# Optimization experiments

Hardware: AMD Instinct MI355X
Metric: run time of the kernel (lower is better)

Reference implementation:

```python
import jax, jax.numpy as jnp
import numpy as np

H = 768   # hidden_dim * SMPL_NR_JOINTS = 32 * 24
O = 72    # output_dim * SMPL_NR_JOINTS = 3 * 24
B = 256
T = 100   # max_len (tgt.size(1))
SRC_LEN = 16


def setup_inputs() -> dict:
    key = jax.random.key(0)
    ks = jax.random.split(key, 10)
    s = 1.0 / np.sqrt(H)
    return {
        "src": jax.random.normal(ks[0], (B, SRC_LEN, H), jnp.float32),
        "tgt": jax.random.normal(ks[1], (B, T, O), jnp.float32),
        "h0": jax.random.normal(ks[2], (B, H), jnp.float32),
        "c0": jax.random.normal(ks[3], (B, H), jnp.float32),
        "W_ih": jax.random.uniform(ks[4], (4 * H, H), jnp.float32, -s, s),
        "W_hh": jax.random.uniform(ks[5], (4 * H, H), jnp.float32, -s, s),
        "b_ih": jax.random.uniform(ks[6], (4 * H,), jnp.float32, -s, s),
        "b_hh": jax.random.uniform(ks[7], (4 * H,), jnp.float32, -s, s),
        "W_post": jax.random.uniform(ks[8], (O, H), jnp.float32, -s, s),
        "b_post": jax.random.uniform(ks[9], (O,), jnp.float32, -s, s),
    }


def reference(src, tgt, h0, c0, W_ih, W_hh, b_ih, b_hh, W_post, b_post):
    max_len = tgt.shape[1]
    bias = b_ih + b_hh  # [4H]

    def step(carry, _):
        x, h, c = carry  # each [B, H]
        gates = x @ W_ih.T + h @ W_hh.T + bias  # [B, 4H]
        i, f, g, o = jnp.split(gates, 4, axis=-1)  # PyTorch gate order i,f,g,o
        c = jax.nn.sigmoid(f) * c + jax.nn.sigmoid(i) * jnp.tanh(g)
        h = jax.nn.sigmoid(o) * jnp.tanh(c)
        return (h, h, c), h  # decoder output feeds back as next input

    x0 = src[:, -1]  # out = src[:, -1].unsqueeze(1)
    _, outs = jax.lax.scan(step, (x0, h0, c0), None, length=max_len)  # [T, B, H]
    outs = jnp.transpose(outs, (1, 0, 2))  # [B, T, H]
    return outs @ W_post.T + b_post  # [B, T, O]
```

## Files before the change

### kernel.cpp

```cpp
#include <hip/hip_runtime.h>
#include <hip/hip_bf16.h>
#include <math.h>

#define H 768
#define B 256
#define T 100

typedef __attribute__((ext_vector_type(8))) short short8;
typedef __attribute__((ext_vector_type(4))) float f32x4;
typedef unsigned long long u64;

static __device__ __forceinline__ float sigm(float x) {
    return 1.0f / (1.0f + __expf(-x));
}
static __device__ __forceinline__ float tanh_fast(float x) {
    return 1.0f - 2.0f / (__expf(2.0f * x) + 1.0f);
}

__global__ void prep_all(const float* __restrict__ src, const float* __restrict__ h0,
                         const float* __restrict__ Wih, const float* __restrict__ Whh,
                         const float* __restrict__ bih, const float* __restrict__ bhh,
                         const float* __restrict__ Wpost,
                         __hip_bfloat16* __restrict__ Wc,
                         __hip_bfloat16* __restrict__ Wcat,
                         float* __restrict__ bias,
                         __hip_bfloat16* __restrict__ Wp,
                         __hip_bfloat16* __restrict__ A0,
                         u64* __restrict__ sig64)
{
    const int bx = blockIdx.x;
    const int y  = blockIdx.y;
    const int k  = bx * 256 + threadIdx.x;
    if (y < 3072) {
        float a = Wih[y * H + k];
        float b = Whh[y * H + k];
        Wc[y * H + k] = __float2bfloat16(a + b);
        Wcat[y * 1536 + k] = __float2bfloat16(a);
        Wcat[y * 1536 + H + k] = __float2bfloat16(b);
        if (bx == 0 && threadIdx.x == 0) bias[y] = bih[y] + bhh[y];
    } else if (y < 3152) {
        int r = y - 3072;
        Wp[r * H + k] = (r < 72) ? __float2bfloat16(Wpost[r * H + k])
                                 : __float2bfloat16(0.0f);
    } else if (y < 3408) {
        int b = y - 3152;
        A0[b * 1536 + k] = __float2bfloat16(src[(b * 16 + 15) * H + k]);
        A0[b * 1536 + H + k] = __float2bfloat16(h0[b * H + k]);
    } else {
        sig64[(size_t)(y - 3408) * 768 + k] = 0ull;
    }
}

#define LDS_H_STRIDE  772
#define LDS_T0_STRIDE 1540
#define XCH_STRIDE    17

#define LDW(nm, idx) \
    asm volatile("global_load_dwordx4 %0, %1, off" \
                 : "=v"(nm) : "v"(wptr + (idx) * 32))

#define KSTEP(nm, idx) { \
    short8 a_ = *(const short8*)(&lds_h[col * LDS_H_STRIDE + (idx) * 32 + quad * 8]); \
    acc = __builtin_amdgcn_mfma_f32_16x16x32_bf16(a_, nm, acc, 0, 0, 0); }

static __device__ __forceinline__ bool sig_ok(u64 x) {
    return (unsigned short)x && (unsigned short)(x >> 16) &&
           (unsigned short)(x >> 32) && (unsigned short)(x >> 48);
}

__global__ __launch_bounds__(768, 3) void lstm_persist(
    const __hip_bfloat16* __restrict__ Wc,
    const __hip_bfloat16* __restrict__ Wcat,
    const float* __restrict__ bias,
    const float* __restrict__ c0in,
    const __hip_bfloat16* __restrict__ A0,
    unsigned* sig)
{
    const int mtg  = blockIdx.x >> 4;
    const int jg   = blockIdx.x & 15;
    const int tid  = threadIdx.x;
    const int lane = tid & 63;
    const int wave = tid >> 6;
    const int col  = lane & 15;
    const int quad = lane >> 4;
    const int jt_l = wave >> 2;
    const int gate = wave & 3;
    const int j    = jg * 48 + jt_l * 16 + col;

    __shared__ short lds_h[16 * LDS_T0_STRIDE];
    __shared__ float xch[12 * 16 * XCH_STRIDE];

    const short* wptr = (const short*)Wc + (size_t)(gate * H + j) * H + quad * 8;
    short8 w00,w01,w02,w03,w04,w05,w06,w07,w08,w09,w10,w11,
           w12,w13,w14,w15,w16,w17,w18,w19,w20,w21,w22,w23;
    LDW(w00,0);  LDW(w01,1);  LDW(w02,2);  LDW(w03,3);
    LDW(w04,4);  LDW(w05,5);  LDW(w06,6);  LDW(w07,7);
    LDW(w08,8);  LDW(w09,9);  LDW(w10,10); LDW(w11,11);
    LDW(w12,12); LDW(w13,13); LDW(w14,14); LDW(w15,15);
    LDW(w16,16); LDW(w17,17); LDW(w18,18); LDW(w19,19);
    LDW(w20,20); LDW(w21,21); LDW(w22,22); LDW(w23,23);
    asm volatile("s_waitcnt vmcnt(0)" ::: "memory");

    const int p    = tid;
    const int bb   = p / 24;
    const int jp   = p % 24;
    const int jloc = jp * 2;
    const int cjt  = jloc >> 4;
    const int jcol = jloc & 15;
    const int bglob = mtg * 16 + bb;
    const int jglob = jg * 48 + jloc;
    float c0v = 0.f, c1v = 0.f;
    float bi0=0,bi1=0,bf0=0,bf1=0,bg0=0,bg1=0,bo0=0,bo1=0;
    if (p < 384) {
        c0v = c0in[(size_t)bglob * H + jglob];
        c1v = c0in[(size_t)bglob * H + jglob + 1];
        bi0 = bias[0*H + jglob]; bi1 = bias[0*H + jglob + 1];
        bf0 = bias[1*H + jglob]; bf1 = bias[1*H + jglob + 1];
        bg0 = bias[2*H + jglob]; bg1 = bias[2*H + jglob + 1];
        bo0 = bias[3*H + jglob]; bo1 = bias[3*H + jglob + 1];
    }

    const u64* sig64c = (const u64*)sig;
    const int r0  = tid / 192;
    const int wrd = tid % 192;

    for (int t = 0; t < T; ++t) {
        f32x4 acc = {0.f, 0.f, 0.f, 0.f};

        if (t == 0) {
            const u64* a8 = (const u64*)((const short*)A0 + (size_t)(mtg * 16) * 1536);
#pragma unroll
            for (int i = 0; i < 8; ++i) {
                int idx = tid + i * 768;
                int br  = idx / 384;
                int ch  = idx % 384;
                *(u64*)&lds_h[br * LDS_T0_STRIDE + ch * 4] = a8[(size_t)br * 384 + ch];
            }
            __syncthreads();

            const short* wq = (const short*)Wcat + (size_t)(gate * H + j) * 1536 + quad * 8;
            for (int kk = 0; kk < 48; ++kk) {
                short8 a_ = *(const short8*)(&lds_h[col * LDS_T0_STRIDE + kk * 32 + quad * 8]);
                short8 b_ = *(const short8*)(wq + kk * 32);
                acc = __builtin_amdgcn_mfma_f32_16x16x32_bf16(a_, b_, acc, 0, 0, 0);
            }
        } else {
            const u64* hb = sig64c + ((size_t)(t - 1) * B + (size_t)(mtg * 16)) * 192;
            unsigned pending = 0xFu;
#pragma unroll
            for (int i = 0; i < 4; ++i) {
                int row = r0 + 4 * i;
                u64 x = __hip_atomic_load(hb + (size_t)row * 192 + wrd,
                                          __ATOMIC_RELAXED, __HIP_MEMORY_SCOPE_AGENT);
                if (sig_ok(x)) {
                    *(u64*)&lds_h[row * LDS_H_STRIDE + wrd * 4] = ~x;
                    pending &= ~(1u << i);
                }
            }
            int guard = 0;
            while (pending && ++guard < (1 << 22)) {
                __builtin_amdgcn_s_sleep(1);
#pragma unroll
                for (int i = 0; i < 4; ++i) {
                    if (pending & (1u << i)) {
                        int row = r0 + 4 * i;
                        u64 x = __hip_atomic_load(hb + (size_t)row * 192 + wrd,
                                                  __ATOMIC_RELAXED, __HIP_MEMORY_SCOPE_AGENT);
                        if (sig_ok(x)) {
                            *(u64*)&lds_h[row * LDS_H_STRIDE + wrd * 4] = ~x;
                            pending &= ~(1u << i);
                        }
                    }
                }
            }
            __syncthreads();

            KSTEP(w00,0)  KSTEP(w01,1)  KSTEP(w02,2)  KSTEP(w03,3)
            KSTEP(w04,4)  KSTEP(w05,5)  KSTEP(w06,6)  KSTEP(w07,7)
            KSTEP(w08,8)  KSTEP(w09,9)  KSTEP(w10,10) KSTEP(w11,11)
            KSTEP(w12,12) KSTEP(w13,13) KSTEP(w14,14) KSTEP(w15,15)
            KSTEP(w16,16) KSTEP(w17,17) KSTEP(w18,18) KSTEP(w19,19)
            KSTEP(w20,20) KSTEP(w21,21) KSTEP(w22,22) KSTEP(w23,23)
        }

        float* xw = &xch[(size_t)wave * 16 * XCH_STRIDE];
#pragma unroll
        for (int r = 0; r < 4; ++r)
            xw[(quad * 4 + r) * XCH_STRIDE + col] = acc[r];
        __syncthreads();

        if (p < 384) {
            const float* xg = &xch[(size_t)(cjt * 4) * 16 * XCH_STRIDE + bb * XCH_STRIDE + jcol];
            const int gs = 16 * XCH_STRIDE;
            float i0 = xg[0*gs] + bi0, i1 = xg[0*gs + 1] + bi1;
            float f0 = xg[1*gs] + bf0, f1 = xg[1*gs + 1] + bf1;
            float g0 = xg[2*gs] + bg0, g1 = xg[2*gs + 1] + bg1;
            float o0 = xg[3*gs] + bo0, o1 = xg[3*gs + 1] + bo1;
            float cn0 = sigm(f0) * c0v + sigm(i0) * tanh_fast(g0);
            float cn1 = sigm(f1) * c1v + sigm(i1) * tanh_fast(g1);
            c0v = cn0; c1v = cn1;
            __hip_bfloat16 h0b = __float2bfloat16(sigm(o0) * tanh_fast(cn0));
            __hip_bfloat16 h1b = __float2bfloat16(sigm(o1) * tanh_fast(cn1));
            unsigned lo = (unsigned)(unsigned short)~(*(unsigned short*)&h0b);
            unsigned hi = (unsigned)(unsigned short)~(*(unsigned short*)&h1b);
            __hip_atomic_store(&sig[((size_t)t * B + bglob) * 384 + (jglob >> 1)],
                               lo | (hi << 16),
                               __ATOMIC_RELAXED, __HIP_MEMORY_SCOPE_AGENT);
        }

        __syncthreads();
    }
}

__global__ __launch_bounds__(64) void proj(
    const short* __restrict__ Hs,
    const __hip_bfloat16* __restrict__ Wp,
    const float* __restrict__ bpost,
    float* __restrict__ out)
{
    const int mt = blockIdx.x;
    const int lane = threadIdx.x;
    const int col = lane & 15;
    const int quad = lane >> 4;

    const short* Ap = Hs + (size_t)(mt * 16 + col) * H + quad * 8;
    const short* Wb = (const short*)Wp;

    f32x4 acc[5];
#pragma unroll
    for (int nt = 0; nt < 5; ++nt) acc[nt] = (f32x4){0.f, 0.f, 0.f, 0.f};

    for (int k = 0; k < H; k += 32) {
        short8 a = ~(*(const short8*)(Ap + k));
#pragma unroll
        for (int nt = 0; nt < 5; ++nt) {
            short8 b = *(const short8*)(Wb + (size_t)(nt * 16 + col) * H + quad * 8 + k);
            acc[nt] = __builtin_amdgcn_mfma_f32_16x16x32_bf16(a, b, acc[nt], 0, 0, 0);
        }
    }

#pragma unroll
    for (int nt = 0; nt < 5; ++nt) {
        const int o = nt * 16 + col;
        if (o < 72) {
            const float bb = bpost[o];
#pragma unroll
            for (int r = 0; r < 4; ++r) {
                const int m = mt * 16 + quad * 4 + r;
                const int t = m >> 8;
                const int b = m & 255;
                out[((size_t)b * T + t) * 72 + o] = acc[nt][r] + bb;
            }
        }
    }
}


extern "C" void kernel_launch(void* const* d_in, const int* in_sizes, int n_in,
                              void* d_out, int out_size, void* d_ws, size_t ws_size,
                              hipStream_t stream) {
    const float* src   = (const float*)d_in[0];
    const float* h0    = (const float*)d_in[2];
    const float* c0    = (const float*)d_in[3];
    const float* Wih   = (const float*)d_in[4];
    const float* Whh   = (const float*)d_in[5];
    const float* bih   = (const float*)d_in[6];
    const float* bhh   = (const float*)d_in[7];
    const float* Wpost = (const float*)d_in[8];
    const float* bpost = (const float*)d_in[9];
    float* out = (float*)d_out;

    char* ws = (char*)d_ws;
    __hip_bfloat16* Wcat = (__hip_bfloat16*)(ws + 0);
    __hip_bfloat16* Wc   = (__hip_bfloat16*)(ws + 9437184);
    float*          bias = (float*)(ws + 14155776);
    __hip_bfloat16* Wp   = (__hip_bfloat16*)(ws + 14168064);
    __hip_bfloat16* A0   = (__hip_bfloat16*)(ws + 14290944);
    unsigned*       sig  = (unsigned*)(ws + 15863808);

    prep_all<<<dim3(3, 9808), 256, 0, stream>>>(src, h0, Wih, Whh, bih, bhh, Wpost,
                                                Wc, Wcat, bias, Wp, A0, (u64*)sig);

    lstm_persist<<<256, 768, 0, stream>>>(Wc, Wcat, bias, c0, A0, sig);

    proj<<<1600, 64, 0, stream>>>((const short*)sig, Wp, bpost, out);
}
```

Baseline: 500.2 us.

## Switch persistent LSTM to 32x32 MFMA tiles with 192-thread blocks

Reworks the persistent LSTM kernel to use 32x32x16 bf16 MFMA instead of 16x16x32. Each block now covers 32 batch rows by 24 hidden units across all four gates using 3 waves, in place of 16 rows by 48 units with 12 waves, and each wave keeps 48 register-resident weight fragments. The cell update now handles 4 batch rows per thread and packs neighbouring outputs with a lane shuffle, and the trailing barrier per step is dropped. This aims to cut per-step MFMA issue and synchronisation overhead, at the cost of higher register pressure, fewer waves per CU and more spin-poll loads per thread. The removed barrier could also let the next step's LDS writes race with reads still in progress.

```diff
diff --git a/kernel.cpp b/kernel.cpp
--- a/kernel.cpp
+++ b/kernel.cpp
@@ -7,6 +7,7 @@
 #define T 100
 
 typedef __attribute__((ext_vector_type(8))) short short8;
+typedef __attribute__((ext_vector_type(16))) float f32x16;
 typedef __attribute__((ext_vector_type(4))) float f32x4;
 typedef unsigned long long u64;
 
@@ -53,22 +54,32 @@
 
 #define LDS_H_STRIDE  772
 #define LDS_T0_STRIDE 1540
-#define XCH_STRIDE    17
-
-#define LDW(nm, idx) \
-    asm volatile("global_load_dwordx4 %0, %1, off" \
-                 : "=v"(nm) : "v"(wptr + (idx) * 32))
-
-#define KSTEP(nm, idx) { \
-    short8 a_ = *(const short8*)(&lds_h[col * LDS_H_STRIDE + (idx) * 32 + quad * 8]); \
-    acc = __builtin_amdgcn_mfma_f32_16x16x32_bf16(a_, nm, acc, 0, 0, 0); }
+#define XCH_STRIDE    33
+
+#define LDW8(n0,n1,n2,n3,n4,n5,n6,n7, p) \
+    asm volatile("global_load_dwordx4 %0, %8, off\n\t" \
+                 "global_load_dwordx4 %1, %8, off offset:32\n\t" \
+                 "global_load_dwordx4 %2, %8, off offset:64\n\t" \
+                 "global_load_dwordx4 %3, %8, off offset:96\n\t" \
+                 "global_load_dwordx4 %4, %8, off offset:128\n\t" \
+                 "global_load_dwordx4 %5, %8, off offset:160\n\t" \
+                 "global_load_dwordx4 %6, %8, off offset:192\n\t" \
+                 "global_load_dwordx4 %7, %8, off offset:224\n\t" \
+                 "s_waitcnt vmcnt(0)" \
+                 : "=&v"(n0),"=&v"(n1),"=&v"(n2),"=&v"(n3), \
+                   "=&v"(n4),"=&v"(n5),"=&v"(n6),"=&v"(n7) \
+                 : "v"(p))
+
+#define KST(nm, idx) { \
+    short8 a_ = *(const short8*)(&lds_h[arow * LDS_H_STRIDE + (idx) * 16 + half * 8]); \
+    acc = __builtin_amdgcn_mfma_f32_32x32x16_bf16(a_, nm, acc, 0, 0, 0); }
 
 static __device__ __forceinline__ bool sig_ok(u64 x) {
     return (unsigned short)x && (unsigned short)(x >> 16) &&
            (unsigned short)(x >> 32) && (unsigned short)(x >> 48);
 }
 
-__global__ __launch_bounds__(768, 3) void lstm_persist(
+__global__ __launch_bounds__(192, 1) void lstm_persist(
     const __hip_bfloat16* __restrict__ Wc,
     const __hip_bfloat16* __restrict__ Wcat,
     const float* __restrict__ bias,
@@ -76,84 +87,79 @@
     const __hip_bfloat16* __restrict__ A0,
     unsigned* sig)
 {
-    const int mtg  = blockIdx.x >> 4;
-    const int jg   = blockIdx.x & 15;
+    const int mtg  = blockIdx.x >> 5;
+    const int jg   = blockIdx.x & 31;
     const int tid  = threadIdx.x;
     const int lane = tid & 63;
     const int wave = tid >> 6;
-    const int col  = lane & 15;
-    const int quad = lane >> 4;
-    const int jt_l = wave >> 2;
-    const int gate = wave & 3;
-    const int j    = jg * 48 + jt_l * 16 + col;
-
-    __shared__ short lds_h[16 * LDS_T0_STRIDE];
-    __shared__ float xch[12 * 16 * XCH_STRIDE];
-
-    const short* wptr = (const short*)Wc + (size_t)(gate * H + j) * H + quad * 8;
+    const int arow = lane & 31;
+    const int half = lane >> 5;
+    const int r    = wave * 32 + arow;
+    const int g    = r / 24;
+    const int j_l  = r % 24;
+    const int Wrow = g * H + jg * 24 + j_l;
+
+    __shared__ short lds_h[32 * LDS_T0_STRIDE];
+    __shared__ float xch[96 * XCH_STRIDE];
+
+    const short* wptr = (const short*)Wc + (size_t)Wrow * H + half * 8;
     short8 w00,w01,w02,w03,w04,w05,w06,w07,w08,w09,w10,w11,
-           w12,w13,w14,w15,w16,w17,w18,w19,w20,w21,w22,w23;
-    LDW(w00,0);  LDW(w01,1);  LDW(w02,2);  LDW(w03,3);
-    LDW(w04,4);  LDW(w05,5);  LDW(w06,6);  LDW(w07,7);
-    LDW(w08,8);  LDW(w09,9);  LDW(w10,10); LDW(w11,11);
-    LDW(w12,12); LDW(w13,13); LDW(w14,14); LDW(w15,15);
-    LDW(w16,16); LDW(w17,17); LDW(w18,18); LDW(w19,19);
-    LDW(w20,20); LDW(w21,21); LDW(w22,22); LDW(w23,23);
-    asm volatile("s_waitcnt vmcnt(0)" ::: "memory");
-
-    const int p    = tid;
-    const int bb   = p / 24;
-    const int jp   = p % 24;
-    const int jloc = jp * 2;
-    const int cjt  = jloc >> 4;
-    const int jcol = jloc & 15;
-    const int bglob = mtg * 16 + bb;
-    const int jglob = jg * 48 + jloc;
-    float c0v = 0.f, c1v = 0.f;
-    float bi0=0,bi1=0,bf0=0,bf1=0,bg0=0,bg1=0,bo0=0,bo1=0;
-    if (p < 384) {
-        c0v = c0in[(size_t)bglob * H + jglob];
-        c1v = c0in[(size_t)bglob * H + jglob + 1];
-        bi0 = bias[0*H + jglob]; bi1 = bias[0*H + jglob + 1];
-        bf0 = bias[1*H + jglob]; bf1 = bias[1*H + jglob + 1];
-        bg0 = bias[2*H + jglob]; bg1 = bias[2*H + jglob + 1];
-        bo0 = bias[3*H + jglob]; bo1 = bias[3*H + jglob + 1];
-    }
+           w12,w13,w14,w15,w16,w17,w18,w19,w20,w21,w22,w23,
+           w24,w25,w26,w27,w28,w29,w30,w31,w32,w33,w34,w35,
+           w36,w37,w38,w39,w40,w41,w42,w43,w44,w45,w46,w47;
+    LDW8(w00,w01,w02,w03,w04,w05,w06,w07, wptr);
+    LDW8(w08,w09,w10,w11,w12,w13,w14,w15, wptr + 128);
+    LDW8(w16,w17,w18,w19,w20,w21,w22,w23, wptr + 256);
+    LDW8(w24,w25,w26,w27,w28,w29,w30,w31, wptr + 384);
+    LDW8(w32,w33,w34,w35,w36,w37,w38,w39, wptr + 512);
+    LDW8(w40,w41,w42,w43,w44,w45,w46,w47, wptr + 640);
+
+    const int cj   = tid % 24;
+    const int cb   = tid / 24;
+    const int jglob = jg * 24 + cj;
+    const int bglob0 = mtg * 32 + cb * 4;
+    const float bi = bias[0 * H + jglob];
+    const float bf = bias[1 * H + jglob];
+    const float bg = bias[2 * H + jglob];
+    const float bo = bias[3 * H + jglob];
+    float cv[4];
+#pragma unroll
+    for (int rr = 0; rr < 4; ++rr)
+        cv[rr] = c0in[(size_t)(bglob0 + rr) * H + jglob];
 
     const u64* sig64c = (const u64*)sig;
-    const int r0  = tid / 192;
-    const int wrd = tid % 192;
 
     for (int t = 0; t < T; ++t) {
-        f32x4 acc = {0.f, 0.f, 0.f, 0.f};
+        f32x16 acc;
+#pragma unroll
+        for (int i = 0; i < 16; ++i) acc[i] = 0.f;
 
         if (t == 0) {
-            const u64* a8 = (const u64*)((const short*)A0 + (size_t)(mtg * 16) * 1536);
-#pragma unroll
-            for (int i = 0; i < 8; ++i) {
-                int idx = tid + i * 768;
+            const u64* a8 = (const u64*)((const short*)A0 + (size_t)(mtg * 32) * 1536);
+#pragma unroll
+            for (int i = 0; i < 64; ++i) {
+                int idx = tid + i * 192;
                 int br  = idx / 384;
                 int ch  = idx % 384;
                 *(u64*)&lds_h[br * LDS_T0_STRIDE + ch * 4] = a8[(size_t)br * 384 + ch];
             }
             __syncthreads();
 
-            const short* wq = (const short*)Wcat + (size_t)(gate * H + j) * 1536 + quad * 8;
-            for (int kk = 0; kk < 48; ++kk) {
-                short8 a_ = *(const short8*)(&lds_h[col * LDS_T0_STRIDE + kk * 32 + quad * 8]);
-                short8 b_ = *(const short8*)(wq + kk * 32);
-                acc = __builtin_amdgcn_mfma_f32_16x16x32_bf16(a_, b_, acc, 0, 0, 0);
+            const short* wq = (const short*)Wcat + (size_t)Wrow * 1536 + half * 8;
+            for (int kk = 0; kk < 96; ++kk) {
+                short8 a_ = *(const short8*)(&lds_h[arow * LDS_T0_STRIDE + kk * 16 + half * 8]);
+                short8 b_ = *(const short8*)(wq + kk * 16);
+                acc = __builtin_amdgcn_mfma_f32_32x32x16_bf16(a_, b_, acc, 0, 0, 0);
             }
         } else {
-            const u64* hb = sig64c + ((size_t)(t - 1) * B + (size_t)(mtg * 16)) * 192;
-            unsigned pending = 0xFu;
-#pragma unroll
-            for (int i = 0; i < 4; ++i) {
-                int row = r0 + 4 * i;
-                u64 x = __hip_atomic_load(hb + (size_t)row * 192 + wrd,
+            const u64* hb = sig64c + ((size_t)(t - 1) * B + (size_t)(mtg * 32)) * 192;
+            unsigned pending = 0xFFFFFFFFu;
+#pragma unroll
+            for (int i = 0; i < 32; ++i) {
+                u64 x = __hip_atomic_load(hb + (size_t)i * 192 + tid,
                                           __ATOMIC_RELAXED, __HIP_MEMORY_SCOPE_AGENT);
                 if (sig_ok(x)) {
-                    *(u64*)&lds_h[row * LDS_H_STRIDE + wrd * 4] = ~x;
+                    *(u64*)&lds_h[i * LDS_H_STRIDE + tid * 4] = ~x;
                     pending &= ~(1u << i);
                 }
             }
@@ -161,13 +167,12 @@
             while (pending && ++guard < (1 << 22)) {
                 __builtin_amdgcn_s_sleep(1);
 #pragma unroll
-                for (int i = 0; i < 4; ++i) {
+                for (int i = 0; i < 32; ++i) {
                     if (pending & (1u << i)) {
-                        int row = r0 + 4 * i;
-                        u64 x = __hip_atomic_load(hb + (size_t)row * 192 + wrd,
+                        u64 x = __hip_atomic_load(hb + (size_t)i * 192 + tid,
                                                   __ATOMIC_RELAXED, __HIP_MEMORY_SCOPE_AGENT);
                         if (sig_ok(x)) {
-                            *(u64*)&lds_h[row * LDS_H_STRIDE + wrd * 4] = ~x;
+                            *(u64*)&lds_h[i * LDS_H_STRIDE + tid * 4] = ~x;
                             pending &= ~(1u << i);
                         }
                     }
@@ -175,40 +180,49 @@
             }
             __syncthreads();
 
-            KSTEP(w00,0)  KSTEP(w01,1)  KSTEP(w02,2)  KSTEP(w03,3)
-            KSTEP(w04,4)  KSTEP(w05,5)  KSTEP(w06,6)  KSTEP(w07,7)
-            KSTEP(w08,8)  KSTEP(w09,9)  KSTEP(w10,10) KSTEP(w11,11)
-            KSTEP(w12,12) KSTEP(w13,13) KSTEP(w14,14) KSTEP(w15,15)
-            KSTEP(w16,16) KSTEP(w17,17) KSTEP(w18,18) KSTEP(w19,19)
-            KSTEP(w20,20) KSTEP(w21,21) KSTEP(w22,22) KSTEP(w23,23)
-        }
-
-        float* xw = &xch[(size_t)wave * 16 * XCH_STRIDE];
-#pragma unroll
-        for (int r = 0; r < 4; ++r)
-            xw[(quad * 4 + r) * XCH_STRIDE + col] = acc[r];
+            KST(w00,0)  KST(w01,1)  KST(w02,2)  KST(w03,3)  KST(w04,4)  KST(w05,5)
+            KST(w06,6)  KST(w07,7)  KST(w08,8)  KST(w09,9)  KST(w10,10) KST(w11,11)
+            KST(w12,12) KST(w13,13) KST(w14,14) KST(w15,15) KST(w16,16) KST(w17,17)
+            KST(w18,18) KST(w19,19) KST(w20,20) KST(w21,21) KST(w22,22) KST(w23,23)
+            KST(w24,24) KST(w25,25) KST(w26,26) KST(w27,27) KST(w28,28) KST(w29,29)
+            KST(w30,30) KST(w31,31) KST(w32,32) KST(w33,33) KST(w34,34) KST(w35,35)
+            KST(w36,36) KST(w37,37) KST(w38,38) KST(w39,39) KST(w40,40) KST(w41,41)
+            KST(w42,42) KST(w43,43) KST(w44,44) KST(w45,45) KST(w46,46) KST(w47,47)
+        }
+
+        {
+            float* xr = &xch[(size_t)r * XCH_STRIDE + 4 * half];
+#pragma unroll
+            for (int reg = 0; reg < 16; ++reg)
+                xr[(reg & 3) + 8 * (reg >> 2)] = acc[reg];
+        }
         __syncthreads();
 
-        if (p < 384) {
-            const float* xg = &xch[(size_t)(cjt * 4) * 16 * XCH_STRIDE + bb * XCH_STRIDE + jcol];
-            const int gs = 16 * XCH_STRIDE;
-            float i0 = xg[0*gs] + bi0, i1 = xg[0*gs + 1] + bi1;
-            float f0 = xg[1*gs] + bf0, f1 = xg[1*gs + 1] + bf1;
-            float g0 = xg[2*gs] + bg0, g1 = xg[2*gs + 1] + bg1;
-            float o0 = xg[3*gs] + bo0, o1 = xg[3*gs + 1] + bo1;
-            float cn0 = sigm(f0) * c0v + sigm(i0) * tanh_fast(g0);
-            float cn1 = sigm(f1) * c1v + sigm(i1) * tanh_fast(g1);
-            c0v = cn0; c1v = cn1;
-            __hip_bfloat16 h0b = __float2bfloat16(sigm(o0) * tanh_fast(cn0));
-            __hip_bfloat16 h1b = __float2bfloat16(sigm(o1) * tanh_fast(cn1));
-            unsigned lo = (unsigned)(unsigned short)~(*(unsigned short*)&h0b);
-            unsigned hi = (unsigned)(unsigned short)~(*(unsigned short*)&h1b);
-            __hip_atomic_store(&sig[((size_t)t * B + bglob) * 384 + (jglob >> 1)],
-                               lo | (hi << 16),
-                               __ATOMIC_RELAXED, __HIP_MEMORY_SCOPE_AGENT);
-        }
-
-        __syncthreads();
+        {
+            unsigned mm[4];
+#pragma unroll
+            for (int rr = 0; rr < 4; ++rr) {
+                const int m = cb * 4 + rr;
+                float i0 = xch[(0 * 24 + cj) * XCH_STRIDE + m] + bi;
+                float f0 = xch[(1 * 24 + cj) * XCH_STRIDE + m] + bf;
+                float g0 = xch[(2 * 24 + cj) * XCH_STRIDE + m] + bg;
+                float o0 = xch[(3 * 24 + cj) * XCH_STRIDE + m] + bo;
+                float cn = sigm(f0) * cv[rr] + sigm(i0) * tanh_fast(g0);
+                cv[rr] = cn;
+                float hn = sigm(o0) * tanh_fast(cn);
+                __hip_bfloat16 hbv = __float2bfloat16(hn);
+                mm[rr] = (unsigned)(unsigned short)~(*(unsigned short*)&hbv);
+            }
+#pragma unroll
+            for (int rr = 0; rr < 4; ++rr) {
+                unsigned other = (unsigned)__shfl_xor((int)mm[rr], 1, 64);
+                if ((cj & 1) == 0) {
+                    __hip_atomic_store(&sig[((size_t)t * B + (bglob0 + rr)) * 384 + (jglob >> 1)],
+                                       mm[rr] | (other << 16),
+                                       __ATOMIC_RELAXED, __HIP_MEMORY_SCOPE_AGENT);
+                }
+            }
+        }
     }
 }
 
@@ -281,7 +295,7 @@
     prep_all<<<dim3(3, 9808), 256, 0, stream>>>(src, h0, Wih, Whh, bih, bhh, Wpost,
                                                 Wc, Wcat, bias, Wp, A0, (u64*)sig);
 
-    lstm_persist<<<256, 768, 0, stream>>>(Wc, Wcat, bias, c0, A0, sig);
+    lstm_persist<<<256, 192, 0, stream>>>(Wc, Wcat, bias, c0, A0, sig);
 
     proj<<<1600, 64, 0, stream>>>((const short*)sig, Wp, bpost, out);
 }
```

Result: slower. 1.463 ms (+192.4%).
